# Optimization experiments

Hardware: AMD Instinct MI355X
Metric: run time of the kernel (lower is better)

The kernel has to match this reference:

```python
import jax, jax.numpy as jnp
import numpy as np

N_POL = 20000; N_COMP = 80000; N = N_POL + N_COMP
E = 1000000; EMB = 128; HID = 256; HEADS = 8; OUT = 128; EA = 5
NEG_SLOPE = 0.2; LN_EPS = 1e-5


def setup_inputs() -> dict:
    ks = jax.random.split(jax.random.key(0), 24)
    def rn(i, shape, s=0.1):
        return jax.random.normal(ks[i], shape, jnp.float32) * s
    C1 = HID // HEADS  # per-head channels of conv1
    return dict(
        pol_feat=rn(0, (N_POL, 7), 1.0),
        state_ids=jax.random.randint(ks[1], (N_POL,), 0, 55),
        comp_cat=jax.random.randint(ks[2], (N_COMP, 2), 0, 16),
        comp_price=rn(3, (N_COMP, 1), 1.0),
        edge_index=jax.random.randint(ks[4], (2, E), 0, N),
        edge_attr=rn(5, (E, EA), 1.0),
        Wp=rn(6, (7, EMB)), bp=jnp.zeros((EMB,), jnp.float32),
        state_emb=rn(7, (55, EMB)), sector_emb=rn(8, (16, 8)), industry_emb=rn(9, (150, 8)),
        Wc=rn(10, (17, EMB)), bc=jnp.zeros((EMB,), jnp.float32),
        ln_g=jnp.ones((EMB,), jnp.float32), ln_b=jnp.zeros((EMB,), jnp.float32),
        W1=rn(11, (EMB, HEADS * C1)), att_src1=rn(12, (HEADS, C1)), att_dst1=rn(13, (HEADS, C1)),
        We1=rn(14, (EA, HEADS * C1)), att_e1=rn(15, (HEADS, C1)), b1=jnp.zeros((HID,), jnp.float32),
        W2=rn(16, (HID, OUT)), att_src2=rn(17, (1, OUT)), att_dst2=rn(18, (1, OUT)),
        We2=rn(19, (EA, OUT)), att_e2=rn(20, (1, OUT)), b2=jnp.zeros((OUT,), jnp.float32),
    )


def _add_self_loops(src, dst, ea, n):
    # PyG add_self_loops with fill_value='mean': self-loop edge_attr = mean of
    # incoming edge attrs per dst node (0 for isolated nodes).
    loop = jnp.arange(n, dtype=src.dtype)
    cnt = jax.ops.segment_sum(jnp.ones(dst.shape, jnp.float32), dst, num_segments=n)
    loop_attr = jax.ops.segment_sum(ea, dst, num_segments=n) / jnp.maximum(cnt, 1.0)[:, None]
    return (jnp.concatenate([src, loop]), jnp.concatenate([dst, loop]),
            jnp.concatenate([ea, loop_attr], 0))


def _gat(x, src, dst, ea, W, a_src, a_dst, We, a_e, bias, concat):
    # PyG GATConv (shared lin for src/dst, edge_dim attention, eval mode).
    n = x.shape[0]
    H, C = a_src.shape
    xw = (x @ W).reshape(n, H, C)                 # [n,H,C]
    al_s = jnp.sum(xw * a_src, -1)                # [n,H]
    al_d = jnp.sum(xw * a_dst, -1)                # [n,H]
    ew = (ea @ We).reshape(-1, H, C)              # [Etot,H,C]
    al_e = jnp.sum(ew * a_e, -1)                  # [Etot,H]
    alpha = jax.nn.leaky_relu(al_s[src] + al_d[dst] + al_e, NEG_SLOPE)
    amax = jax.ops.segment_max(alpha, dst, num_segments=n)
    ex = jnp.exp(alpha - amax[dst])
    denom = jax.ops.segment_sum(ex, dst, num_segments=n)
    alpha = ex / (denom[dst] + 1e-16)             # segment softmax over dst
    out = jax.ops.segment_sum(xw[src] * alpha[:, :, None], dst, num_segments=n)
    out = out.reshape(n, H * C) if concat else out.mean(1)
    return out + bias


def reference(pol_feat, state_ids, comp_cat, comp_price, edge_index, edge_attr,
              Wp, bp, state_emb, sector_emb, industry_emb, Wc, bc, ln_g, ln_b,
              W1, att_src1, att_dst1, We1, att_e1, b1,
              W2, att_src2, att_dst2, We2, att_e2, b2):
    pol = jax.nn.relu(pol_feat @ Wp + bp) + state_emb[state_ids]
    comp_in = jnp.concatenate([sector_emb[comp_cat[:, 0]], industry_emb[comp_cat[:, 1]], comp_price], 1)
    comp = jax.nn.relu(comp_in @ Wc + bc)
    x = jnp.concatenate([pol, comp], 0)           # [N,EMB]
    mu = jnp.mean(x, -1, keepdims=True)
    var = jnp.var(x, -1, keepdims=True)
    x = (x - mu) / jnp.sqrt(var + LN_EPS) * ln_g + ln_b
    src, dst, ea = _add_self_loops(edge_index[0], edge_index[1], edge_attr, x.shape[0])
    h = jax.nn.elu(_gat(x, src, dst, ea, W1, att_src1, att_dst1, We1, att_e1, b1, True))
    return _gat(h, src, dst, ea, W2, att_src2, att_dst2, We2, att_e2, b2, False)
```

## Files before the change

kernel.cpp:

```cpp
#include <hip/hip_runtime.h>
#include <hip/hip_fp16.h>
#include <math.h>

#define N_POL 20000
#define N_COMP 80000
#define NN (N_POL + N_COMP)
#define EE 1000000
#define NB1 ((NN + 1023) / 1024)

typedef short bf16x8 __attribute__((ext_vector_type(8)));
typedef float f32x4 __attribute__((ext_vector_type(4)));

struct __align__(16) PEdge {
  int s;
  float ale2;
  unsigned short a1[8];
  unsigned pad[2];
};

__device__ __forceinline__ float wave_sum(float v) {
#pragma unroll
  for (int o = 32; o > 0; o >>= 1) v += __shfl_xor(v, o);
  return v;
}
__device__ __forceinline__ float wave_max(float v) {
#pragma unroll
  for (int o = 32; o > 0; o >>= 1) v = fmaxf(v, __shfl_xor(v, o));
  return v;
}
__device__ __forceinline__ unsigned short f2bf(float f) {
  unsigned b = __float_as_uint(f);
  return (unsigned short)((b + 0x7FFFu + ((b >> 16) & 1u)) >> 16);
}
__device__ __forceinline__ float bf2f(unsigned short u) {
  return __uint_as_float(((unsigned)u) << 16);
}
__device__ __forceinline__ unsigned short f2h(float f) {
  __half h = __float2half_rn(f);
  return *(unsigned short*)&h;
}
__device__ __forceinline__ float h2f(unsigned short u) {
  __half h = *(__half*)&u;
  return __half2float(h);
}

__global__ void k_pre(const float* W2, const float* as2, const float* ad2,
                      const float* We1, const float* ae1, const float* We2,
                      const float* ae2, float* us2, float* ud2, float* V1, float* V2) {
  int t = threadIdx.x;
  if (t < 256) {
    float s = 0.f, d = 0.f;
    for (int c = 0; c < 128; c++) {
      float w = W2[t * 128 + c];
      s = fmaf(w, as2[c], s);
      d = fmaf(w, ad2[c], d);
    }
    us2[t] = s; ud2[t] = d;
  }
  if (t < 40) {
    int k = t >> 3, h = t & 7;
    float v = 0.f;
    for (int c = 0; c < 32; c++) v = fmaf(We1[k * 256 + h * 32 + c], ae1[h * 32 + c], v);
    V1[k * 8 + h] = v;
  }
  if (t < 5) {
    float v = 0.f;
    for (int c = 0; c < 128; c++) v = fmaf(We2[t * 128 + c], ae2[c], v);
    V2[t] = v;
  }
}

__global__ void k_prew(const float* W1, const float* W2, unsigned short* W1t,
                       unsigned short* W2t) {
  int id = blockIdx.x * 256 + threadIdx.x;
  if (id < 32768) {
    int n = id >> 7, k = id & 127;
    W1t[id] = f2bf(W1[k * 256 + n]);
  } else {
    int id2 = id - 32768;
    int n = id2 >> 8, k = id2 & 255;
    W2t[id2] = f2bf(W2[k * 128 + n]);
  }
}

__global__ __launch_bounds__(256) void k_encode(
    const float* pol_feat, const int* state_ids, const int* comp_cat,
    const float* comp_price, const float* Wp, const float* bp,
    const float* state_emb, const float* sector_emb, const float* industry_emb,
    const float* Wc, const float* bc, const float* ln_g, const float* ln_b,
    unsigned short* x) {
  int t = threadIdx.x;
  int i = blockIdx.x * 2 + (t >> 7), c = t & 127;
  float v;
  if (i < N_POL) {
    float acc = bp[c];
#pragma unroll
    for (int k = 0; k < 7; k++) acc = fmaf(pol_feat[i * 7 + k], Wp[k * 128 + c], acc);
    v = fmaxf(acc, 0.f) + state_emb[state_ids[i] * 128 + c];
  } else {
    int j = i - N_POL;
    int sc = comp_cat[2 * j], in = comp_cat[2 * j + 1];
    float acc = bc[c];
#pragma unroll
    for (int k = 0; k < 8; k++) acc = fmaf(sector_emb[sc * 8 + k], Wc[k * 128 + c], acc);
#pragma unroll
    for (int k = 0; k < 8; k++) acc = fmaf(industry_emb[in * 8 + k], Wc[(8 + k) * 128 + c], acc);
    acc = fmaf(comp_price[j], Wc[16 * 128 + c], acc);
    v = fmaxf(acc, 0.f);
  }
  __shared__ float red[4];
  int wid = t >> 6, lane = t & 63;
  int base = (t >> 7) << 1;
  float s = wave_sum(v);
  if (lane == 0) red[wid] = s;
  __syncthreads();
  float mu = (red[base] + red[base + 1]) * (1.f / 128.f);
  float t0 = v - mu;
  __syncthreads();
  float s2 = wave_sum(t0 * t0);
  if (lane == 0) red[wid] = s2;
  __syncthreads();
  float var = (red[base] + red[base + 1]) * (1.f / 128.f);
  float r = rsqrtf(var + 1e-5f);
  float xf = t0 * r * ln_g[c] + ln_b[c];
  x[(size_t)i * 128 + c] = f2bf(xf);
}

__global__ void k_hist(const int* dst, unsigned* hist) {
  int e = blockIdx.x * blockDim.x + threadIdx.x;
  if (e < EE) atomicAdd(&hist[dst[e]], 1u);
}
__global__ __launch_bounds__(1024) void k_scan1(const unsigned* hist, unsigned* rowptr,
                                                unsigned* part) {
  __shared__ unsigned sc[1024];
  int t = threadIdx.x;
  int i = blockIdx.x * 1024 + t;
  unsigned v = (i < NN) ? hist[i] : 0u;
  sc[t] = v;
  __syncthreads();
  for (int o = 1; o < 1024; o <<= 1) {
    unsigned add = (t >= o) ? sc[t - o] : 0u;
    __syncthreads();
    sc[t] += add;
    __syncthreads();
  }
  if (i < NN) rowptr[i] = sc[t] - v;
  if (t == 1023) part[blockIdx.x] = sc[1023];
}
__global__ void k_scan2(unsigned* part) {
  if (threadIdx.x == 0) {
    unsigned run = 0;
    for (int b = 0; b < NB1; b++) { unsigned t = part[b]; part[b] = run; run += t; }
  }
}
__global__ void k_scan3(unsigned* rowptr, const unsigned* part, unsigned* cursor) {
  int i = blockIdx.x * blockDim.x + threadIdx.x;
  if (i < NN) {
    unsigned r = rowptr[i] + part[i >> 10];
    rowptr[i] = r;
    cursor[i] = r;
  }
  if (i == 0) rowptr[NN] = EE;
}
__global__ void k_scatter(const int* src, const int* dst, const float* ea,
                          const float* V1, const float* V2, unsigned* cursor,
                          PEdge* ep) {
  int e = blockIdx.x * blockDim.x + threadIdx.x;
  if (e >= EE) return;
  int d = dst[e];
  unsigned pos = atomicAdd(&cursor[d], 1u);
  float av[5];
#pragma unroll
  for (int k = 0; k < 5; k++) av[k] = ea[(size_t)e * 5 + k];
  float a2 = 0.f;
#pragma unroll
  for (int k = 0; k < 5; k++) a2 = fmaf(av[k], V2[k], a2);
  unsigned short hb[8];
#pragma unroll
  for (int hh = 0; hh < 8; hh++) {
    float a1 = 0.f;
#pragma unroll
    for (int k = 0; k < 5; k++) a1 = fmaf(av[k], V1[k * 8 + hh], a1);
    hb[hh] = f2h(a1);
  }
  uint4 w0, w1;
  w0.x = (unsigned)src[e];
  w0.y = __float_as_uint(a2);
  w0.z = (unsigned)hb[0] | ((unsigned)hb[1] << 16);
  w0.w = (unsigned)hb[2] | ((unsigned)hb[3] << 16);
  w1.x = (unsigned)hb[4] | ((unsigned)hb[5] << 16);
  w1.y = (unsigned)hb[6] | ((unsigned)hb[7] << 16);
  w1.z = 0u; w1.w = 0u;
  uint4* p = (uint4*)(ep + pos);
  p[0] = w0;
  p[1] = w1;
}

__global__ __launch_bounds__(256) void k_gemm1(const unsigned short* x,
                                               const unsigned short* W1t,
                                               unsigned short* xw1) {
  __shared__ char wlds[65536];
  int tid = threadIdx.x;
#pragma unroll
  for (int it = 0; it < 16; it++) {
    int cch = it * 256 + tid;
    int row = cch >> 4, seg = cch & 15;
    uint4 v = *(const uint4*)(W1t + row * 128 + seg * 8);
    *(uint4*)(&wlds[(row * 256 + seg * 16) ^ ((row & 7) << 4)]) = v;
  }
  __syncthreads();
  int wid = tid >> 6, l = tid & 63;
  int cl = l & 15, kh = l >> 4;
  int swz = (cl & 7) << 4;
  long r0 = (long)blockIdx.x * 128 + wid * 32;
  f32x4 acc[2][16];
#pragma unroll
  for (int rt = 0; rt < 2; rt++)
#pragma unroll
    for (int nt = 0; nt < 16; nt++) acc[rt][nt] = {0.f, 0.f, 0.f, 0.f};
  long ra0 = r0 + cl; if (ra0 > NN - 1) ra0 = NN - 1;
  long ra1 = r0 + 16 + cl; if (ra1 > NN - 1) ra1 = NN - 1;
#pragma unroll
  for (int kk = 0; kk < 4; kk++) {
    bf16x8 a0 = *(const bf16x8*)(x + ra0 * 128 + kk * 32 + kh * 8);
    bf16x8 a1 = *(const bf16x8*)(x + ra1 * 128 + kk * 32 + kh * 8);
#pragma unroll
    for (int nt = 0; nt < 16; nt++) {
      bf16x8 b = *(const bf16x8*)(&wlds[(((nt * 16 + cl) * 256) + kk * 64 + kh * 16) ^ swz]);
      acc[0][nt] = __builtin_amdgcn_mfma_f32_16x16x32_bf16(a0, b, acc[0][nt], 0, 0, 0);
      acc[1][nt] = __builtin_amdgcn_mfma_f32_16x16x32_bf16(a1, b, acc[1][nt], 0, 0, 0);
    }
  }
#pragma unroll
  for (int rt = 0; rt < 2; rt++)
#pragma unroll
    for (int nt = 0; nt < 16; nt++)
#pragma unroll
      for (int j = 0; j < 4; j++) {
        long row = r0 + rt * 16 + kh * 4 + j;
        if (row < NN) xw1[row * 256 + nt * 16 + cl] = f2bf(acc[rt][nt][j]);
      }
}

__global__ __launch_bounds__(256) void k_al(const unsigned short* xw1, const float* as1,
                                            const float* ad1, float* al_s1,
                                            float* al_d1) {
  int w = threadIdx.x >> 6, lane = threadIdx.x & 63;
  int i = blockIdx.x * 4 + w;
  if (i >= NN) return;
  ushort4 xv = ((const ushort4*)(xw1 + (size_t)i * 256))[lane];
  float4 as = ((const float4*)as1)[lane];
  float4 ad = ((const float4*)ad1)[lane];
  float x0 = bf2f(xv.x), x1 = bf2f(xv.y), x2 = bf2f(xv.z), x3 = bf2f(xv.w);
  float s = x0 * as.x + x1 * as.y + x2 * as.z + x3 * as.w;
  float d = x0 * ad.x + x1 * ad.y + x2 * ad.z + x3 * ad.w;
#pragma unroll
  for (int o = 1; o < 8; o <<= 1) {
    s += __shfl_xor(s, o);
    d += __shfl_xor(d, o);
  }
  if ((lane & 7) == 0) {
    al_s1[i * 8 + (lane >> 3)] = s;
    al_d1[i * 8 + (lane >> 3)] = d;
  }
}

__global__ __launch_bounds__(256) void k_gemm2(const unsigned short* h,
                                               const unsigned short* W2t,
                                               unsigned short* xw2) {
  __shared__ char wlds[65536];
  int tid = threadIdx.x;
#pragma unroll
  for (int it = 0; it < 16; it++) {
    int cch = it * 256 + tid;
    int row = cch >> 5, seg = cch & 31;
    uint4 v = *(const uint4*)(W2t + row * 256 + seg * 8);
    *(uint4*)(&wlds[(row * 512 + seg * 16) ^ ((row & 7) << 4)]) = v;
  }
  __syncthreads();
  int wid = tid >> 6, l = tid & 63;
  int cl = l & 15, kh = l >> 4;
  int swz = (cl & 7) << 4;
  long r0 = (long)blockIdx.x * 128 + wid * 32;
  f32x4 acc[2][8];
#pragma unroll
  for (int rt = 0; rt < 2; rt++)
#pragma unroll
    for (int nt = 0; nt < 8; nt++) acc[rt][nt] = {0.f, 0.f, 0.f, 0.f};
  long ra0 = r0 + cl; if (ra0 > NN - 1) ra0 = NN - 1;
  long ra1 = r0 + 16 + cl; if (ra1 > NN - 1) ra1 = NN - 1;
#pragma unroll
  for (int kk = 0; kk < 8; kk++) {
    bf16x8 a0 = *(const bf16x8*)(h + ra0 * 256 + kk * 32 + kh * 8);
    bf16x8 a1 = *(const bf16x8*)(h + ra1 * 256 + kk * 32 + kh * 8);
#pragma unroll
    for (int nt = 0; nt < 8; nt++) {
      bf16x8 b = *(const bf16x8*)(&wlds[(((nt * 16 + cl) * 512) + kk * 64 + kh * 16) ^ swz]);
      acc[0][nt] = __builtin_amdgcn_mfma_f32_16x16x32_bf16(a0, b, acc[0][nt], 0, 0, 0);
      acc[1][nt] = __builtin_amdgcn_mfma_f32_16x16x32_bf16(a1, b, acc[1][nt], 0, 0, 0);
    }
  }
#pragma unroll
  for (int rt = 0; rt < 2; rt++)
#pragma unroll
    for (int nt = 0; nt < 8; nt++)
#pragma unroll
      for (int j = 0; j < 4; j++) {
        long row = r0 + rt * 16 + kh * 4 + j;
        if (row < NN) xw2[row * 128 + nt * 16 + cl] = f2bf(acc[rt][nt][j]);
      }
}

__global__ __launch_bounds__(256) void k_gat1(
    const unsigned* rowptr, const PEdge* ep, const float* al_s1, const float* al_d1,
    const unsigned short* xw1, const float* b1, const float* us2, const float* ud2,
    unsigned short* h, float* al_s2, float* al_d2) {
  int w = threadIdx.x >> 6, lane = threadIdx.x & 63;
  int i = blockIdx.x * 4 + w;
  if (i >= NN) return;
  int r0 = rowptr[i], r1 = rowptr[i + 1];
  int hh = lane & 7;
  int js = lane >> 3;
  int ah = lane >> 3;
  float ald = al_d1[i * 8 + hh];
  float m = -1e30f, l = 0.f;
  float a0 = 0.f, a1 = 0.f, a2 = 0.f, a3 = 0.f;
  float alesum = 0.f;

  auto chunk = [&](int jb, int cnt) {
    bool valid = js < cnt;
    int jc = jb + (valid ? js : cnt - 1);
    int s = ((const int*)&ep[jc])[0];
    float ale = h2f(((const unsigned short*)&ep[jc])[4 + hh]);
    if (!valid) ale = 0.f;
    alesum += ale;
    float logit = -1e30f;
    if (valid) {
      float al = al_s1[s * 8 + hh] + ald + ale;
      logit = al > 0.f ? al : 0.2f * al;
    }
    float cm = logit;
    cm = fmaxf(cm, __shfl_xor(cm, 8));
    cm = fmaxf(cm, __shfl_xor(cm, 16));
    cm = fmaxf(cm, __shfl_xor(cm, 32));
    float mn = fmaxf(m, cm);
    float sc = __expf(m - mn);
    float p = __expf(logit - mn);
    float ps = p;
    ps += __shfl_xor(ps, 8);
    ps += __shfl_xor(ps, 16);
    ps += __shfl_xor(ps, 32);
    l = l * sc + ps;
    m = mn;
    float asc = __shfl(sc, ah);
    a0 *= asc; a1 *= asc; a2 *= asc; a3 *= asc;
    for (int jj = 0; jj < cnt; jj++) {
      float pj = __shfl(p, jj * 8 + ah);
      int sj = __shfl(s, jj * 8);
      ushort4 xv = ((const ushort4*)(xw1 + (size_t)sj * 256))[lane];
      a0 = fmaf(pj, bf2f(xv.x), a0);
      a1 = fmaf(pj, bf2f(xv.y), a1);
      a2 = fmaf(pj, bf2f(xv.z), a2);
      a3 = fmaf(pj, bf2f(xv.w), a3);
    }
  };
  int jb = r0;
  for (; jb + 8 <= r1; jb += 8) chunk(jb, 8);
  if (jb < r1) chunk(jb, r1 - jb);

  alesum += __shfl_xor(alesum, 8);
  alesum += __shfl_xor(alesum, 16);
  alesum += __shfl_xor(alesum, 32);
  float inv = 1.f / fmaxf((float)(r1 - r0), 1.f);
  float aleS = alesum * inv;
  {
    float al = al_s1[i * 8 + hh] + ald + aleS;
    float logit = al > 0.f ? al : 0.2f * al;
    float mn = fmaxf(m, logit);
    float sc = __expf(m - mn);
    float p = __expf(logit - mn);
    l = l * sc + p;
    m = mn;
    float asc = __shfl(sc, ah);
    float pj = __shfl(p, ah);
    ushort4 xv = ((const ushort4*)(xw1 + (size_t)i * 256))[lane];
    a0 = fmaf(pj, bf2f(xv.x), a0 * asc);
    a1 = fmaf(pj, bf2f(xv.y), a1 * asc);
    a2 = fmaf(pj, bf2f(xv.z), a2 * asc);
    a3 = fmaf(pj, bf2f(xv.w), a3 * asc);
  }
  float lh = __shfl(l, ah);
  float invl = 1.f / (lh + 1e-16f);
  float4 bv = ((const float4*)b1)[lane];
  float v0 = a0 * invl + bv.x, v1 = a1 * invl + bv.y;
  float v2 = a2 * invl + bv.z, v3 = a3 * invl + bv.w;
  v0 = v0 > 0.f ? v0 : expm1f(v0);
  v1 = v1 > 0.f ? v1 : expm1f(v1);
  v2 = v2 > 0.f ? v2 : expm1f(v2);
  v3 = v3 > 0.f ? v3 : expm1f(v3);
  ushort4 hv;
  hv.x = f2bf(v0); hv.y = f2bf(v1); hv.z = f2bf(v2); hv.w = f2bf(v3);
  ((ushort4*)(h + (size_t)i * 256))[lane] = hv;
  float4 uv = ((const float4*)us2)[lane];
  float4 dv = ((const float4*)ud2)[lane];
  float ps2 = v0 * uv.x + v1 * uv.y + v2 * uv.z + v3 * uv.w;
  float pd2 = v0 * dv.x + v1 * dv.y + v2 * dv.z + v3 * dv.w;
  ps2 = wave_sum(ps2);
  pd2 = wave_sum(pd2);
  if (lane == 0) { al_s2[i] = ps2; al_d2[i] = pd2; }
}

__global__ __launch_bounds__(256) void k_gat2(
    const unsigned* rowptr, const PEdge* ep, const float* al_s2, const float* al_d2,
    const unsigned short* xw2, const float* b2, float* out) {
  int w = threadIdx.x >> 6, lane = threadIdx.x & 63;
  int i = blockIdx.x * 4 + w;
  if (i >= NN) return;
  int r0 = rowptr[i], r1 = rowptr[i + 1];
  float ald = al_d2[i];
  float m = -1e30f, l = 0.f, a0 = 0.f, a1 = 0.f;
  float alesum = 0.f;

  auto chunk = [&](int jb, int cnt) {
    bool valid = lane < cnt;
    int jc = jb + (valid ? lane : cnt - 1);
    int2 sv = *(const int2*)&ep[jc];
    int s = sv.x;
    float ale = valid ? __uint_as_float((unsigned)sv.y) : 0.f;
    alesum += ale;
    float logit = -1e30f;
    if (valid) {
      float al = al_s2[s] + ald + ale;
      logit = al > 0.f ? al : 0.2f * al;
    }
    float cm = wave_max(logit);
    float mn = fmaxf(m, cm);
    float sc = __expf(m - mn);
    float p = __expf(logit - mn);
    float ps = wave_sum(p);
    l = l * sc + ps;
    m = mn;
    a0 *= sc; a1 *= sc;
    for (int jj = 0; jj < cnt; jj++) {
      float pj = __shfl(p, jj);
      int sj = __shfl(s, jj);
      ushort2 xv = ((const ushort2*)(xw2 + (size_t)sj * 128))[lane];
      a0 = fmaf(pj, bf2f(xv.x), a0);
      a1 = fmaf(pj, bf2f(xv.y), a1);
    }
  };
  int jb = r0;
  for (; jb + 64 <= r1; jb += 64) chunk(jb, 64);
  if (jb < r1) chunk(jb, r1 - jb);

  alesum = wave_sum(alesum);
  float inv = 1.f / fmaxf((float)(r1 - r0), 1.f);
  float aleS = alesum * inv;
  {
    float al = al_s2[i] + ald + aleS;
    float logit = al > 0.f ? al : 0.2f * al;
    float mn = fmaxf(m, logit);
    float sc = __expf(m - mn);
    float p = __expf(logit - mn);
    l = l * sc + p;
    ushort2 xv = ((const ushort2*)(xw2 + (size_t)i * 128))[lane];
    a0 = fmaf(p, bf2f(xv.x), a0 * sc);
    a1 = fmaf(p, bf2f(xv.y), a1 * sc);
  }
  float invl = 1.f / (l + 1e-16f);
  float2 bv = ((const float2*)b2)[lane];
  float2 ov = {a0 * invl + bv.x, a1 * invl + bv.y};
  ((float2*)(out + (size_t)i * 128))[lane] = ov;
}

extern "C" void kernel_launch(void* const* d_in, const int* in_sizes, int n_in,
                              void* d_out, int out_size, void* d_ws, size_t ws_size,
                              hipStream_t stream) {
  const float* pol_feat = (const float*)d_in[0];
  const int* state_ids = (const int*)d_in[1];
  const int* comp_cat = (const int*)d_in[2];
  const float* comp_price = (const float*)d_in[3];
  const int* edge_index = (const int*)d_in[4];
  const float* edge_attr = (const float*)d_in[5];
  const float* Wp = (const float*)d_in[6];
  const float* bp = (const float*)d_in[7];
  const float* state_emb = (const float*)d_in[8];
  const float* sector_emb = (const float*)d_in[9];
  const float* industry_emb = (const float*)d_in[10];
  const float* Wc = (const float*)d_in[11];
  const float* bc = (const float*)d_in[12];
  const float* ln_g = (const float*)d_in[13];
  const float* ln_b = (const float*)d_in[14];
  const float* W1 = (const float*)d_in[15];
  const float* as1 = (const float*)d_in[16];
  const float* ad1 = (const float*)d_in[17];
  const float* We1 = (const float*)d_in[18];
  const float* ae1 = (const float*)d_in[19];
  const float* b1 = (const float*)d_in[20];
  const float* W2 = (const float*)d_in[21];
  const float* as2 = (const float*)d_in[22];
  const float* ad2 = (const float*)d_in[23];
  const float* We2 = (const float*)d_in[24];
  const float* ae2 = (const float*)d_in[25];
  const float* b2 = (const float*)d_in[26];
  const int* srcv = edge_index;
  const int* dstv = edge_index + EE;
  float* out = (float*)d_out;

  size_t off = 0;
  auto alloc = [&](size_t nbytes) -> char* {
    char* p = (char*)d_ws + off;
    off += ((nbytes + 255) & ~(size_t)255);
    return p;
  };
  char* regA = alloc((size_t)NN * 512);
  char* regB = alloc((size_t)NN * 512);
  unsigned short* xw1 = (unsigned short*)regA;
  unsigned short* xw2 = (unsigned short*)regA;
  unsigned short* h = (unsigned short*)regB;
  unsigned short* x = (unsigned short*)regB;
  float* al_s1 = (float*)alloc((size_t)NN * 8 * 4);
  float* al_d1 = (float*)alloc((size_t)NN * 8 * 4);
  float* al_s2 = (float*)alloc((size_t)NN * 4);
  float* al_d2 = (float*)alloc((size_t)NN * 4);
  float* us2 = (float*)alloc(256 * 4);
  float* ud2 = (float*)alloc(256 * 4);
  float* V1 = (float*)alloc(64 * 4);
  float* V2 = (float*)alloc(8 * 4);
  unsigned short* W1t = (unsigned short*)alloc(32768 * 2);
  unsigned short* W2t = (unsigned short*)alloc(32768 * 2);
  unsigned* hist = (unsigned*)alloc((size_t)NN * 4);
  unsigned* rowptr = (unsigned*)alloc((size_t)(NN + 1) * 4);
  unsigned* cursor = (unsigned*)alloc((size_t)NN * 4);
  unsigned* part = (unsigned*)alloc((size_t)NB1 * 4);
  PEdge* ep = (PEdge*)alloc((size_t)EE * sizeof(PEdge));

  hipMemsetAsync(hist, 0, (size_t)NN * 4, stream);

  k_pre<<<1, 256, 0, stream>>>(W2, as2, ad2, We1, ae1, We2, ae2, us2, ud2, V1, V2);
  k_prew<<<256, 256, 0, stream>>>(W1, W2, W1t, W2t);
  k_encode<<<NN / 2, 256, 0, stream>>>(pol_feat, state_ids, comp_cat, comp_price, Wp,
                                       bp, state_emb, sector_emb, industry_emb, Wc, bc,
                                       ln_g, ln_b, x);
  k_hist<<<(EE + 255) / 256, 256, 0, stream>>>(dstv, hist);
  k_scan1<<<NB1, 1024, 0, stream>>>(hist, rowptr, part);
  k_scan2<<<1, 64, 0, stream>>>(part);
  k_scan3<<<(NN + 255) / 256, 256, 0, stream>>>(rowptr, part, cursor);
  k_scatter<<<(EE + 255) / 256, 256, 0, stream>>>(srcv, dstv, edge_attr, V1, V2,
                                                  cursor, ep);
  k_gemm1<<<(NN + 127) / 128, 256, 0, stream>>>(x, W1t, xw1);
  k_al<<<NN / 4, 256, 0, stream>>>(xw1, as1, ad1, al_s1, al_d1);
  k_gat1<<<NN / 4, 256, 0, stream>>>(rowptr, ep, al_s1, al_d1, xw1, b1, us2, ud2, h,
                                     al_s2, al_d2);
  k_gemm2<<<(NN + 127) / 128, 256, 0, stream>>>(h, W2t, xw2);
  k_gat2<<<NN / 4, 256, 0, stream>>>(rowptr, ep, al_s2, al_d2, xw2, b2, out);
}
```

Measured before the change: 444.2 us.

## Fuse prep kernels, precompute embedding tables, unroll GAT edge loops, use exp2

Merges the two weight-prep kernels into one launch. That kernel also precomputes the sector and industry embedding-times-Wc tables, so the encoder does two table lookups instead of 16 FMAs per channel. Attention logits are pre-scaled by log2(e) so the softmax can use exp2f. The layer-1 gather processes 16 edges per step and the layer-2 full chunks issue eight row loads at once, both to raise memory-level parallelism. The serial scan over block partials becomes a parallel shared-memory scan; the unrolled paths add register pressure.

```diff
diff --git a/kernel.cpp b/kernel.cpp
--- a/kernel.cpp
+++ b/kernel.cpp
@@ -7,6 +7,7 @@
 #define NN (N_POL + N_COMP)
 #define EE 1000000
 #define NB1 ((NN + 1023) / 1024)
+#define LOG2E 1.44269504f
 
 typedef short bf16x8 __attribute__((ext_vector_type(8)));
 typedef float f32x4 __attribute__((ext_vector_type(4)));
@@ -44,51 +45,65 @@
   return __half2float(h);
 }
 
-__global__ void k_pre(const float* W2, const float* as2, const float* ad2,
-                      const float* We1, const float* ae1, const float* We2,
-                      const float* ae2, float* us2, float* ud2, float* V1, float* V2) {
-  int t = threadIdx.x;
-  if (t < 256) {
+__global__ __launch_bounds__(256) void k_prep(
+    const float* W1, const float* W2, const float* as2, const float* ad2,
+    const float* We1, const float* ae1, const float* We2, const float* ae2,
+    const float* sector_emb, const float* industry_emb, const float* Wc,
+    unsigned short* W1t, unsigned short* W2t, float* Ts, float* Ti, float* us2,
+    float* ud2, float* V1, float* V2) {
+  int id = blockIdx.x * 256 + threadIdx.x;
+  if (id < 32768) {
+    int n = id >> 7, k = id & 127;
+    W1t[id] = f2bf(W1[k * 256 + n]);
+  } else if (id < 65536) {
+    int id2 = id - 32768;
+    int n = id2 >> 8, k = id2 & 255;
+    W2t[id2] = f2bf(W2[k * 128 + n]);
+  } else if (id < 67584) {
+    int id2 = id - 65536;
+    int n = id2 >> 7, c = id2 & 127;
+    float a = 0.f;
+#pragma unroll
+    for (int k = 0; k < 8; k++) a = fmaf(sector_emb[n * 8 + k], Wc[k * 128 + c], a);
+    Ts[id2] = a;
+  } else if (id < 86784) {
+    int id2 = id - 67584;
+    int n = id2 >> 7, c = id2 & 127;
+    float a = 0.f;
+#pragma unroll
+    for (int k = 0; k < 8; k++) a = fmaf(industry_emb[n * 8 + k], Wc[(8 + k) * 128 + c], a);
+    Ti[id2] = a;
+  } else if (id < 87040) {
+    int t = id - 86784;
     float s = 0.f, d = 0.f;
     for (int c = 0; c < 128; c++) {
       float w = W2[t * 128 + c];
       s = fmaf(w, as2[c], s);
       d = fmaf(w, ad2[c], d);
     }
-    us2[t] = s; ud2[t] = d;
-  }
-  if (t < 40) {
+    us2[t] = s * LOG2E;
+    ud2[t] = d * LOG2E;
+  } else if (id < 87104) {
+    int t = id - 87040;
     int k = t >> 3, h = t & 7;
-    float v = 0.f;
-    for (int c = 0; c < 32; c++) v = fmaf(We1[k * 256 + h * 32 + c], ae1[h * 32 + c], v);
-    V1[k * 8 + h] = v;
-  }
-  if (t < 5) {
+    if (k < 5) {
+      float v = 0.f;
+      for (int c = 0; c < 32; c++) v = fmaf(We1[k * 256 + h * 32 + c], ae1[h * 32 + c], v);
+      V1[k * 8 + h] = v * LOG2E;
+    }
+  } else if (id < 87109) {
+    int t = id - 87104;
     float v = 0.f;
     for (int c = 0; c < 128; c++) v = fmaf(We2[t * 128 + c], ae2[c], v);
-    V2[t] = v;
-  }
-}
-
-__global__ void k_prew(const float* W1, const float* W2, unsigned short* W1t,
-                       unsigned short* W2t) {
-  int id = blockIdx.x * 256 + threadIdx.x;
-  if (id < 32768) {
-    int n = id >> 7, k = id & 127;
-    W1t[id] = f2bf(W1[k * 256 + n]);
-  } else {
-    int id2 = id - 32768;
-    int n = id2 >> 8, k = id2 & 255;
-    W2t[id2] = f2bf(W2[k * 128 + n]);
+    V2[t] = v * LOG2E;
   }
 }
 
 __global__ __launch_bounds__(256) void k_encode(
     const float* pol_feat, const int* state_ids, const int* comp_cat,
-    const float* comp_price, const float* Wp, const float* bp,
-    const float* state_emb, const float* sector_emb, const float* industry_emb,
-    const float* Wc, const float* bc, const float* ln_g, const float* ln_b,
-    unsigned short* x) {
+    const float* comp_price, const float* Wp, const float* bp, const float* state_emb,
+    const float* Ts, const float* Ti, const float* Wc, const float* bc,
+    const float* ln_g, const float* ln_b, unsigned short* x) {
   int t = threadIdx.x;
   int i = blockIdx.x * 2 + (t >> 7), c = t & 127;
   float v;
@@ -100,12 +115,8 @@
   } else {
     int j = i - N_POL;
     int sc = comp_cat[2 * j], in = comp_cat[2 * j + 1];
-    float acc = bc[c];
-#pragma unroll
-    for (int k = 0; k < 8; k++) acc = fmaf(sector_emb[sc * 8 + k], Wc[k * 128 + c], acc);
-#pragma unroll
-    for (int k = 0; k < 8; k++) acc = fmaf(industry_emb[in * 8 + k], Wc[(8 + k) * 128 + c], acc);
-    acc = fmaf(comp_price[j], Wc[16 * 128 + c], acc);
+    float acc = Ts[sc * 128 + c] + Ti[in * 128 + c] +
+                comp_price[j] * Wc[16 * 128 + c] + bc[c];
     v = fmaxf(acc, 0.f);
   }
   __shared__ float red[4];
@@ -147,11 +158,19 @@
   if (i < NN) rowptr[i] = sc[t] - v;
   if (t == 1023) part[blockIdx.x] = sc[1023];
 }
-__global__ void k_scan2(unsigned* part) {
-  if (threadIdx.x == 0) {
-    unsigned run = 0;
-    for (int b = 0; b < NB1; b++) { unsigned t = part[b]; part[b] = run; run += t; }
-  }
+__global__ __launch_bounds__(128) void k_scan2(unsigned* part) {
+  __shared__ unsigned sc[128];
+  int t = threadIdx.x;
+  unsigned v = (t < NB1) ? part[t] : 0u;
+  sc[t] = v;
+  __syncthreads();
+  for (int o = 1; o < 128; o <<= 1) {
+    unsigned add = (t >= o) ? sc[t - o] : 0u;
+    __syncthreads();
+    sc[t] += add;
+    __syncthreads();
+  }
+  if (t < NB1) part[t] = sc[t] - v;
 }
 __global__ void k_scan3(unsigned* rowptr, const unsigned* part, unsigned* cursor) {
   int i = blockIdx.x * blockDim.x + threadIdx.x;
@@ -260,8 +279,8 @@
     d += __shfl_xor(d, o);
   }
   if ((lane & 7) == 0) {
-    al_s1[i * 8 + (lane >> 3)] = s;
-    al_d1[i * 8 + (lane >> 3)] = d;
+    al_s1[i * 8 + (lane >> 3)] = s * LOG2E;
+    al_d1[i * 8 + (lane >> 3)] = d * LOG2E;
   }
 }
 
@@ -327,10 +346,58 @@
   float a0 = 0.f, a1 = 0.f, a2 = 0.f, a3 = 0.f;
   float alesum = 0.f;
 
-  auto chunk = [&](int jb, int cnt) {
+  auto chunk16 = [&](int jb) {
+    int jc0 = jb + js, jc1 = jb + 8 + js;
+    int s0 = *(const int*)&ep[jc0];
+    int s1 = *(const int*)&ep[jc1];
+    float e0 = h2f(((const unsigned short*)&ep[jc0])[4 + hh]);
+    float e1 = h2f(((const unsigned short*)&ep[jc1])[4 + hh]);
+    alesum += e0 + e1;
+    float g0 = al_s1[s0 * 8 + hh] + ald + e0;
+    g0 = g0 > 0.f ? g0 : 0.2f * g0;
+    float g1 = al_s1[s1 * 8 + hh] + ald + e1;
+    g1 = g1 > 0.f ? g1 : 0.2f * g1;
+    float cm = fmaxf(g0, g1);
+    cm = fmaxf(cm, __shfl_xor(cm, 8));
+    cm = fmaxf(cm, __shfl_xor(cm, 16));
+    cm = fmaxf(cm, __shfl_xor(cm, 32));
+    float mn = fmaxf(m, cm);
+    float sc = exp2f(m - mn);
+    float p0 = exp2f(g0 - mn), p1 = exp2f(g1 - mn);
+    float ps = p0 + p1;
+    ps += __shfl_xor(ps, 8);
+    ps += __shfl_xor(ps, 16);
+    ps += __shfl_xor(ps, 32);
+    l = l * sc + ps;
+    m = mn;
+    float asc = __shfl(sc, ah);
+    a0 *= asc; a1 *= asc; a2 *= asc; a3 *= asc;
+#pragma unroll
+    for (int jj = 0; jj < 8; jj++) {
+      float pj = __shfl(p0, jj * 8 + ah);
+      int sj = __shfl(s0, jj * 8);
+      ushort4 xv = ((const ushort4*)(xw1 + (size_t)sj * 256))[lane];
+      a0 = fmaf(pj, bf2f(xv.x), a0);
+      a1 = fmaf(pj, bf2f(xv.y), a1);
+      a2 = fmaf(pj, bf2f(xv.z), a2);
+      a3 = fmaf(pj, bf2f(xv.w), a3);
+    }
+#pragma unroll
+    for (int jj = 0; jj < 8; jj++) {
+      float pj = __shfl(p1, jj * 8 + ah);
+      int sj = __shfl(s1, jj * 8);
+      ushort4 xv = ((const ushort4*)(xw1 + (size_t)sj * 256))[lane];
+      a0 = fmaf(pj, bf2f(xv.x), a0);
+      a1 = fmaf(pj, bf2f(xv.y), a1);
+      a2 = fmaf(pj, bf2f(xv.z), a2);
+      a3 = fmaf(pj, bf2f(xv.w), a3);
+    }
+  };
+
+  auto chunk8 = [&](int jb, int cnt) {
     bool valid = js < cnt;
     int jc = jb + (valid ? js : cnt - 1);
-    int s = ((const int*)&ep[jc])[0];
+    int s = *(const int*)&ep[jc];
     float ale = h2f(((const unsigned short*)&ep[jc])[4 + hh]);
     if (!valid) ale = 0.f;
     alesum += ale;
@@ -344,8 +411,8 @@
     cm = fmaxf(cm, __shfl_xor(cm, 16));
     cm = fmaxf(cm, __shfl_xor(cm, 32));
     float mn = fmaxf(m, cm);
-    float sc = __expf(m - mn);
-    float p = __expf(logit - mn);
+    float sc = exp2f(m - mn);
+    float p = exp2f(logit - mn);
     float ps = p;
     ps += __shfl_xor(ps, 8);
     ps += __shfl_xor(ps, 16);
@@ -364,9 +431,11 @@
       a3 = fmaf(pj, bf2f(xv.w), a3);
     }
   };
+
   int jb = r0;
-  for (; jb + 8 <= r1; jb += 8) chunk(jb, 8);
-  if (jb < r1) chunk(jb, r1 - jb);
+  for (; jb + 16 <= r1; jb += 16) chunk16(jb);
+  if (jb + 8 <= r1) { chunk8(jb, 8); jb += 8; }
+  if (jb < r1) chunk8(jb, r1 - jb);
 
   alesum += __shfl_xor(alesum, 8);
   alesum += __shfl_xor(alesum, 16);
@@ -377,8 +446,8 @@
     float al = al_s1[i * 8 + hh] + ald + aleS;
     float logit = al > 0.f ? al : 0.2f * al;
     float mn = fmaxf(m, logit);
-    float sc = __expf(m - mn);
-    float p = __expf(logit - mn);
+    float sc = exp2f(m - mn);
+    float p = exp2f(logit - mn);
     l = l * sc + p;
     m = mn;
     float asc = __shfl(sc, ah);
@@ -421,6 +490,51 @@
   float m = -1e30f, l = 0.f, a0 = 0.f, a1 = 0.f;
   float alesum = 0.f;
 
+  auto chunkF = [&](int jb) {
+    int jc = jb + lane;
+    int2 sv = *(const int2*)&ep[jc];
+    int s = sv.x;
+    float ale = __uint_as_float((unsigned)sv.y);
+    alesum += ale;
+    float al = al_s2[s] + ald + ale;
+    float logit = al > 0.f ? al : 0.2f * al;
+    float cm = wave_max(logit);
+    float mn = fmaxf(m, cm);
+    float sc = exp2f(m - mn);
+    float p = exp2f(logit - mn);
+    float ps = wave_sum(p);
+    l = l * sc + ps;
+    m = mn;
+    a0 *= sc; a1 *= sc;
+#pragma unroll
+    for (int g = 0; g < 8; g++) {
+      float pj0 = __shfl(p, g * 8 + 0); int sj0 = __shfl(s, g * 8 + 0);
+      float pj1 = __shfl(p, g * 8 + 1); int sj1 = __shfl(s, g * 8 + 1);
+      float pj2 = __shfl(p, g * 8 + 2); int sj2 = __shfl(s, g * 8 + 2);
+      float pj3 = __shfl(p, g * 8 + 3); int sj3 = __shfl(s, g * 8 + 3);
+      float pj4 = __shfl(p, g * 8 + 4); int sj4 = __shfl(s, g * 8 + 4);
+      float pj5 = __shfl(p, g * 8 + 5); int sj5 = __shfl(s, g * 8 + 5);
+      float pj6 = __shfl(p, g * 8 + 6); int sj6 = __shfl(s, g * 8 + 6);
+      float pj7 = __shfl(p, g * 8 + 7); int sj7 = __shfl(s, g * 8 + 7);
+      ushort2 x0 = ((const ushort2*)(xw2 + (size_t)sj0 * 128))[lane];
+      ushort2 x1 = ((const ushort2*)(xw2 + (size_t)sj1 * 128))[lane];
+      ushort2 x2 = ((const ushort2*)(xw2 + (size_t)sj2 * 128))[lane];
+      ushort2 x3 = ((const ushort2*)(xw2 + (size_t)sj3 * 128))[lane];
+      ushort2 x4 = ((const ushort2*)(xw2 + (size_t)sj4 * 128))[lane];
+      ushort2 x5 = ((const ushort2*)(xw2 + (size_t)sj5 * 128))[lane];
+      ushort2 x6 = ((const ushort2*)(xw2 + (size_t)sj6 * 128))[lane];
+      ushort2 x7 = ((const ushort2*)(xw2 + (size_t)sj7 * 128))[lane];
+      a0 = fmaf(pj0, bf2f(x0.x), a0); a1 = fmaf(pj0, bf2f(x0.y), a1);
+      a0 = fmaf(pj1, bf2f(x1.x), a0); a1 = fmaf(pj1, bf2f(x1.y), a1);
+      a0 = fmaf(pj2, bf2f(x2.x), a0); a1 = fmaf(pj2, bf2f(x2.y), a1);
+      a0 = fmaf(pj3, bf2f(x3.x), a0); a1 = fmaf(pj3, bf2f(x3.y), a1);
+      a0 = fmaf(pj4, bf2f(x4.x), a0); a1 = fmaf(pj4, bf2f(x4.y), a1);
+      a0 = fmaf(pj5, bf2f(x5.x), a0); a1 = fmaf(pj5, bf2f(x5.y), a1);
+      a0 = fmaf(pj6, bf2f(x6.x), a0); a1 = fmaf(pj6, bf2f(x6.y), a1);
+      a0 = fmaf(pj7, bf2f(x7.x), a0); a1 = fmaf(pj7, bf2f(x7.y), a1);
+    }
+  };
+
   auto chunk = [&](int jb, int cnt) {
     bool valid = lane < cnt;
     int jc = jb + (valid ? lane : cnt - 1);
@@ -435,8 +549,8 @@
     }
     float cm = wave_max(logit);
     float mn = fmaxf(m, cm);
-    float sc = __expf(m - mn);
-    float p = __expf(logit - mn);
+    float sc = exp2f(m - mn);
+    float p = exp2f(logit - mn);
     float ps = wave_sum(p);
     l = l * sc + ps;
     m = mn;
@@ -449,8 +563,9 @@
       a1 = fmaf(pj, bf2f(xv.y), a1);
     }
   };
+
   int jb = r0;
-  for (; jb + 64 <= r1; jb += 64) chunk(jb, 64);
+  for (; jb + 64 <= r1; jb += 64) chunkF(jb);
   if (jb < r1) chunk(jb, r1 - jb);
 
   alesum = wave_sum(alesum);
@@ -460,8 +575,8 @@
     float al = al_s2[i] + ald + aleS;
     float logit = al > 0.f ? al : 0.2f * al;
     float mn = fmaxf(m, logit);
-    float sc = __expf(m - mn);
-    float p = __expf(logit - mn);
+    float sc = exp2f(m - mn);
+    float p = exp2f(logit - mn);
     l = l * sc + p;
     ushort2 xv = ((const ushort2*)(xw2 + (size_t)i * 128))[lane];
     a0 = fmaf(p, bf2f(xv.x), a0 * sc);
@@ -527,6 +642,8 @@
   float* ud2 = (float*)alloc(256 * 4);
   float* V1 = (float*)alloc(64 * 4);
   float* V2 = (float*)alloc(8 * 4);
+  float* Ts = (float*)alloc(16 * 128 * 4);
+  float* Ti = (float*)alloc(150 * 128 * 4);
   unsigned short* W1t = (unsigned short*)alloc(32768 * 2);
   unsigned short* W2t = (unsigned short*)alloc(32768 * 2);
   unsigned* hist = (unsigned*)alloc((size_t)NN * 4);
@@ -537,14 +654,13 @@
 
   hipMemsetAsync(hist, 0, (size_t)NN * 4, stream);
 
-  k_pre<<<1, 256, 0, stream>>>(W2, as2, ad2, We1, ae1, We2, ae2, us2, ud2, V1, V2);
-  k_prew<<<256, 256, 0, stream>>>(W1, W2, W1t, W2t);
+  k_prep<<<341, 256, 0, stream>>>(W1, W2, as2, ad2, We1, ae1, We2, ae2, sector_emb,
+                                  industry_emb, Wc, W1t, W2t, Ts, Ti, us2, ud2, V1, V2);
   k_encode<<<NN / 2, 256, 0, stream>>>(pol_feat, state_ids, comp_cat, comp_price, Wp,
-                                       bp, state_emb, sector_emb, industry_emb, Wc, bc,
-                                       ln_g, ln_b, x);
+                                       bp, state_emb, Ts, Ti, Wc, bc, ln_g, ln_b, x);
   k_hist<<<(EE + 255) / 256, 256, 0, stream>>>(dstv, hist);
   k_scan1<<<NB1, 1024, 0, stream>>>(hist, rowptr, part);
-  k_scan2<<<1, 64, 0, stream>>>(part);
+  k_scan2<<<1, 128, 0, stream>>>(part);
   k_scan3<<<(NN + 255) / 256, 256, 0, stream>>>(rowptr, part, cursor);
   k_scatter<<<(EE + 255) / 256, 256, 0, stream>>>(srcv, dstv, edge_attr, V1, V2,
                                                   cursor, ep);
```

New measurement: 541.9 us. +22.0%, slower.
